# Kernel optimization log

Hardware: AMD Instinct MI355X
Metric: run time of the kernel (lower is better)

The kernel has to match this reference:

```python
import jax, jax.numpy as jnp
import numpy as np

D_MODEL = 1024
NUM_HEADS = 16
D_HEAD = D_MODEL // NUM_HEADS
ROPE_THETA = 10000.0


def _rope(x, pos):
    # x: [..., S, d_head]; rotate consecutive pairs (2i, 2i+1)
    half = x.shape[-1] // 2
    inv_freq = ROPE_THETA ** (-jnp.arange(half, dtype=jnp.float32) * 2.0 / x.shape[-1])
    ang = pos[:, None].astype(jnp.float32) * inv_freq[None, :]  # [S, half]
    cos, sin = jnp.cos(ang), jnp.sin(ang)
    x1, x2 = x[..., 0::2], x[..., 1::2]
    r1 = x1 * cos - x2 * sin
    r2 = x1 * sin + x2 * cos
    return jnp.stack([r1, r2], axis=-1).reshape(x.shape)


def setup_inputs() -> dict:
    key = jax.random.key(0)
    ks = jax.random.split(key, 5)
    s = 1.0 / np.sqrt(D_MODEL)
    return {
        "q_weight": jax.random.normal(ks[0], (D_MODEL, D_MODEL), jnp.float32) * s,
        "k_weight": jax.random.normal(ks[1], (D_MODEL, D_MODEL), jnp.float32) * s,
        "v_weight": jax.random.normal(ks[2], (D_MODEL, D_MODEL), jnp.float32) * s,
        "o_weight": jax.random.normal(ks[3], (D_MODEL, D_MODEL), jnp.float32) * s,
        "in_features": jax.random.normal(ks[4], (2, 2048, D_MODEL), jnp.float32),
    }


def reference(q_weight, k_weight, v_weight, o_weight, in_features):
    S = in_features.shape[-2]
    qw = q_weight.reshape(NUM_HEADS, D_HEAD, D_MODEL)
    kw = k_weight.reshape(NUM_HEADS, D_HEAD, D_MODEL)
    vw = v_weight.reshape(NUM_HEADS, D_HEAD, D_MODEL)
    # [B, H, S, d_head]
    q = jnp.einsum('bsj,nhj->bnsh', in_features, qw)
    k = jnp.einsum('bsj,nhj->bnsh', in_features, kw)
    v = jnp.einsum('bsj,nhj->bnsh', in_features, vw)
    pos = jnp.arange(S)
    q = _rope(q, pos)
    k = _rope(k, pos)
    scale = 1.0 / jnp.sqrt(jnp.asarray(D_HEAD, dtype=q.dtype))
    scores = jnp.einsum('bnqh,bnkh->bnqk', q, k) * scale  # [B,H,S,S]
    causal = jnp.tril(jnp.ones((S, S), dtype=bool))
    scores = jnp.where(causal, scores, jnp.asarray(-jnp.inf, dtype=scores.dtype))
    attn = jax.nn.softmax(scores, axis=-1)
    out = jnp.einsum('bnqk,bnkh->bnqh', attn, v)  # [B,H,S,d_head]
    out = jnp.swapaxes(out, -2, -3).reshape(*out.shape[:-3], S, D_MODEL)
    return jnp.einsum('ji,bki->bkj', o_weight, out)
```

## Files before the change

kernel.cpp:

```cpp
#include <hip/hip_runtime.h>
#include <math.h>

typedef __attribute__((ext_vector_type(8))) short bf16x8;
typedef __attribute__((ext_vector_type(4))) float f32x4;

static constexpr int D_MODEL = 1024;
static constexpr int SEQ = 2048;
static constexpr int BATCH = 2;
static constexpr int M_TOT = BATCH * SEQ;

__device__ __forceinline__ unsigned short f2bf(float f) {
  unsigned int u = __builtin_bit_cast(unsigned int, f);
  u += 0x7fffu + ((u >> 16) & 1u);
  return (unsigned short)(u >> 16);
}

__device__ __forceinline__ void gld16(const unsigned short* g, unsigned short* l) {
  __builtin_amdgcn_global_load_lds(
      (const __attribute__((address_space(1))) unsigned int*)g,
      (__attribute__((address_space(3))) unsigned int*)l, 16, 0, 0);
}

__global__ void cvt_f32_bf16(const float* __restrict__ src,
                             unsigned short* __restrict__ dst, int n4) {
  int i = blockIdx.x * blockDim.x + threadIdx.x;
  if (i >= n4) return;
  const float4 v = reinterpret_cast<const float4*>(src)[i];
  ushort4 o;
  o.x = f2bf(v.x); o.y = f2bf(v.y); o.z = f2bf(v.z); o.w = f2bf(v.w);
  reinterpret_cast<ushort4*>(dst)[i] = o;
}

__global__ void cvt_weights(const float* __restrict__ qw, const float* __restrict__ kw,
                            const float* __restrict__ vw, const float* __restrict__ ow,
                            unsigned short* __restrict__ dst) {
  int i = blockIdx.x * blockDim.x + threadIdx.x;
  const int which = i >> 18;
  const int off = i & 262143;
  const float* src = (which == 0) ? qw : (which == 1) ? kw : (which == 2) ? vw : ow;
  const float4 v = reinterpret_cast<const float4*>(src)[off];
  ushort4 o;
  o.x = f2bf(v.x); o.y = f2bf(v.y); o.z = f2bf(v.z); o.w = f2bf(v.w);
  reinterpret_cast<ushort4*>(dst)[i] = o;
}

__global__ void rope_tables(float2* __restrict__ ct2) {
  int idx = blockIdx.x * blockDim.x + threadIdx.x;
  int s = idx >> 5;
  int p = idx & 31;
  float inv_freq = powf(10000.0f, -(float)p / 32.0f);
  float ang = (float)s * inv_freq;
  int psw = p ^ (((s >> 2) & 1) << 3);
  float2 cs; cs.x = cosf(ang); cs.y = sinf(ang);
  ct2[s * 32 + psw] = cs;
}

template <int BM, int BN, int MODE>
__global__ __launch_bounds__(256, 2)
void gemm2(const unsigned short* __restrict__ A,
           const unsigned short* __restrict__ W,
           unsigned short* __restrict__ Qd,
           unsigned short* __restrict__ Kd,
           unsigned short* __restrict__ Vd,
           float* __restrict__ Fd,
           const float2* __restrict__ ct2) {
  constexpr int MI = BM / 32, NI = BN / 32;
  constexpr int NKT = D_MODEL / 32;
  constexpr int LOADS = BM / 64 + BN / 64;
  __shared__ __align__(16) unsigned short smem[2 * (BM + BN) * 32];
  unsigned short* Asm = smem;
  unsigned short* Bsm = smem + 2 * BM * 32;
  const int tid  = threadIdx.x;
  const int lane = tid & 63;
  const int wave = tid >> 6;
  const int wm = wave >> 1, wn = wave & 1;
  const int m0 = blockIdx.y * BM;
  const int n0 = blockIdx.x * BN;
  const int lr = lane & 15, lg = lane >> 4;

  const int srow = lane >> 2;
  const int scol = ((lane & 3) ^ ((lane >> 3) & 3)) * 8;

  auto stage = [&](int buf, int kt) {
    const int k0 = kt * 32;
#pragma unroll
    for (int rr = 0; rr < BM / 64; ++rr) {
      const int ch = rr * 4 + wave;
      gld16(&A[(size_t)(m0 + ch * 16 + srow) * D_MODEL + k0 + scol], &Asm[buf * BM * 32 + ch * 512]);
    }
#pragma unroll
    for (int rr = 0; rr < BN / 64; ++rr) {
      const int ch = rr * 4 + wave;
      gld16(&W[(size_t)(n0 + ch * 16 + srow) * D_MODEL + k0 + scol], &Bsm[buf * BN * 32 + ch * 512]);
    }
  };

  f32x4 acc[MI][NI] = {};

  stage(0, 0);
  stage(1, 1);
  __builtin_amdgcn_sched_barrier(0);

  const int swz = (lg ^ ((lr >> 1) & 3)) * 8;

  for (int kt = 0; kt < NKT; ++kt) {
    const int cur = kt & 1;
    if (kt + 1 < NKT) {
      if constexpr (LOADS == 4) asm volatile("s_waitcnt vmcnt(4)" ::: "memory");
      else                      asm volatile("s_waitcnt vmcnt(3)" ::: "memory");
    } else {
      asm volatile("s_waitcnt vmcnt(0)" ::: "memory");
    }
    __builtin_amdgcn_s_barrier();
    __builtin_amdgcn_sched_barrier(0);

    bf16x8 af[MI], bfr[NI];
#pragma unroll
    for (int i = 0; i < MI; ++i)
      af[i] = *reinterpret_cast<const bf16x8*>(&Asm[cur * BM * 32 + (wm * (BM / 2) + i * 16 + lr) * 32 + swz]);
#pragma unroll
    for (int j = 0; j < NI; ++j)
      bfr[j] = *reinterpret_cast<const bf16x8*>(&Bsm[cur * BN * 32 + (wn * (BN / 2) + j * 16 + lr) * 32 + swz]);
    asm volatile("s_waitcnt lgkmcnt(0)" ::: "memory");
    __builtin_amdgcn_sched_barrier(0);
    __builtin_amdgcn_s_barrier();
    __builtin_amdgcn_sched_barrier(0);

    if (kt + 2 < NKT) stage(cur, kt + 2);
    __builtin_amdgcn_sched_barrier(0);

#pragma unroll
    for (int i = 0; i < MI; ++i)
#pragma unroll
      for (int j = 0; j < NI; ++j)
        acc[i][j] = __builtin_amdgcn_mfma_f32_16x16x32_bf16(af[i], bfr[j], acc[i][j], 0, 0, 0);
  }

  if constexpr (MODE == 2) {
#pragma unroll
    for (int i = 0; i < MI; ++i)
#pragma unroll
      for (int j = 0; j < NI; ++j)
#pragma unroll
        for (int r = 0; r < 4; ++r) {
          const int gm = m0 + wm * (BM / 2) + i * 16 + lg * 4 + r;
          const int gc = n0 + wn * (BN / 2) + j * 16 + lr;
          Fd[(size_t)gm * D_MODEL + gc] = acc[i][j][r];
        }
  } else {
    const int t = n0 >> 10;
    const int b = m0 >> 11;
    const int s_base = m0 & 2047;
    if (t < 2) {
      unsigned short* dstQ = (t == 0) ? Qd : Kd;
      const unsigned short* gsrc = (const unsigned short*)(ct2 + (size_t)s_base * 32);
#pragma unroll
      for (int it = 0; it < 8; ++it) {
        const int ch = wave * 8 + it;
        gld16(&gsrc[ch * 512 + lane * 8], &smem[ch * 512]);
      }
      asm volatile("s_waitcnt vmcnt(0)" ::: "memory");
      __builtin_amdgcn_sched_barrier(0);
      __builtin_amdgcn_s_barrier();
      const float2* tbl = (const float2*)smem;
      const int nbase = (n0 & 1023) >> 6;
#pragma unroll
      for (int i = 0; i < MI; ++i) {
#pragma unroll
        for (int j = 0; j < NI; ++j) {
#pragma unroll
          for (int r = 0; r < 4; ++r) {
            const int sl = wm * (BM / 2) + i * 16 + lg * 4 + r;
            const int h  = j * 16 + lr;
            const int psw = (h >> 1) ^ (((sl >> 2) & 1) << 3);
            const float2 cs = tbl[sl * 32 + psw];
            float x = acc[i][j][r];
            const float part = __shfl_xor(x, 1, 64);
            x = (h & 1) ? (part * cs.y + x * cs.x) : (x * cs.x - part * cs.y);
            const int n = nbase + wn;
            dstQ[(size_t)((b * 16 + n) * SEQ + s_base + sl) * 64 + h] = f2bf(x);
          }
        }
      }
    } else {
      unsigned short* tile = smem;
      const int row = tid >> 2;
      const int ck  = tid & 3;
      for (int pass = 0; pass < 2; ++pass) {
        __builtin_amdgcn_s_barrier();
        if (wn == pass) {
#pragma unroll
          for (int i = 0; i < MI; ++i)
#pragma unroll
            for (int j = 0; j < NI; ++j)
#pragma unroll
              for (int r = 0; r < 4; ++r)
                tile[(j * 16 + lr) * 136 + wm * 64 + i * 16 + lg * 4 + r] = f2bf(acc[i][j][r]);
        }
        asm volatile("s_waitcnt lgkmcnt(0)" ::: "memory");
        __builtin_amdgcn_sched_barrier(0);
        __builtin_amdgcn_s_barrier();
        const int c = (n0 & 1023) + pass * 64 + row;
        const int n = c >> 6, h = c & 63;
        unsigned short* vrow = &Vd[(size_t)((b * 16 + n) * 64 + h) * SEQ + s_base + ck * 32];
        const unsigned short* lrow = &tile[row * 136 + ck * 32];
#pragma unroll
        for (int k = 0; k < 4; ++k)
          *reinterpret_cast<bf16x8*>(&vrow[k * 8]) = *reinterpret_cast<const bf16x8*>(&lrow[k * 8]);
      }
    }
  }
}

__global__ __launch_bounds__(256, 2)
void attn_kernel(const unsigned short* __restrict__ Q,
                 const unsigned short* __restrict__ K,
                 const unsigned short* __restrict__ Vt,
                 unsigned short* __restrict__ AO) {
  __shared__ __align__(16) unsigned short Ksh[2][4096];
  __shared__ __align__(16) unsigned short Vsh[2][4096];
  __shared__ unsigned short Pl[4][32 * 72];
  const int bn   = blockIdx.x;
  const int j    = (gridDim.y - 1) - blockIdx.y;
  const int wave = threadIdx.x >> 6;
  const int lane = threadIdx.x & 63;
  const int lr = lane & 15, lg = lane >> 4;
  const int q0 = j * 128 + wave * 32;
  const unsigned short* Qh = Q  + (size_t)bn * SEQ * 64;
  const unsigned short* Kh = K  + (size_t)bn * SEQ * 64;
  const unsigned short* Vh = Vt + (size_t)bn * 64 * SEQ;
  unsigned short* Pw = &Pl[wave][0];
  const int b = bn >> 4, n = bn & 15;

  const int srow8 = lane >> 3;
  const int scolb = ((lane & 7) ^ srow8) * 8;

  auto stage = [&](int buf, int k0) {
#pragma unroll
    for (int c = 0; c < 2; ++c) {
      const int ch = wave * 2 + c;
      const int row = ch * 8 + srow8;
      gld16(&Kh[(size_t)(k0 + row) * 64 + scolb], &Ksh[buf][ch * 512]);
      gld16(&Vh[(size_t)row * SEQ + k0 + scolb], &Vsh[buf][ch * 512]);
    }
  };

  constexpr float KL2E = 0.125f * 1.44269504088896f;
  const int nt = 2 * j + 2;

  bf16x8 qf[2][2];
#pragma unroll
  for (int mi = 0; mi < 2; ++mi)
#pragma unroll
    for (int ks = 0; ks < 2; ++ks)
      qf[mi][ks] = *reinterpret_cast<const bf16x8*>(
          &Qh[(size_t)(q0 + mi * 16 + lr) * 64 + ks * 32 + lg * 8]);
  asm volatile("s_waitcnt vmcnt(0)" ::: "memory");
  __builtin_amdgcn_sched_barrier(0);

  f32x4 o[2][4] = {};
  float lsum[2][4] = {};

  stage(0, 0);
  stage(1, 64);
  __builtin_amdgcn_sched_barrier(0);

  for (int t = 0; t < nt; ++t) {
    const int cur = t & 1;
    const int k0 = t * 64;
    if (t + 1 < nt) { asm volatile("s_waitcnt vmcnt(4)" ::: "memory"); }
    else            { asm volatile("s_waitcnt vmcnt(0)" ::: "memory"); }
    __builtin_amdgcn_s_barrier();
    __builtin_amdgcn_sched_barrier(0);

    const unsigned short* Kc = &Ksh[cur][0];
    const unsigned short* Vc = &Vsh[cur][0];

    bf16x8 kf[4][2];
#pragma unroll
    for (int nj = 0; nj < 4; ++nj)
#pragma unroll
      for (int ks = 0; ks < 2; ++ks) {
        const int R = nj * 16 + lr;
        const int p = (ks * 4 + lg) ^ (R & 7);
        kf[nj][ks] = *reinterpret_cast<const bf16x8*>(&Kc[R * 64 + p * 8]);
      }
    f32x4 sf[2][4] = {};
    __builtin_amdgcn_s_setprio(1);
#pragma unroll
    for (int nj = 0; nj < 4; ++nj)
#pragma unroll
      for (int ks = 0; ks < 2; ++ks)
#pragma unroll
        for (int mi = 0; mi < 2; ++mi)
          sf[mi][nj] = __builtin_amdgcn_mfma_f32_16x16x32_bf16(qf[mi][ks], kf[nj][ks], sf[mi][nj], 0, 0, 0);
    __builtin_amdgcn_s_setprio(0);

    if (k0 + 63 <= q0) {
#pragma unroll
      for (int mi = 0; mi < 2; ++mi)
#pragma unroll
        for (int nj = 0; nj < 4; ++nj)
#pragma unroll
          for (int r = 0; r < 4; ++r) {
            const float p = __builtin_amdgcn_exp2f(sf[mi][nj][r] * KL2E);
            lsum[mi][r] += p;
            Pw[(mi * 16 + lg * 4 + r) * 72 + nj * 16 + lr] = f2bf(p);
          }
    } else {
#pragma unroll
      for (int mi = 0; mi < 2; ++mi)
#pragma unroll
        for (int nj = 0; nj < 4; ++nj)
#pragma unroll
          for (int r = 0; r < 4; ++r) {
            const int qrow = q0 + mi * 16 + lg * 4 + r;
            const int kcol = k0 + nj * 16 + lr;
            const float p = (kcol <= qrow) ? __builtin_amdgcn_exp2f(sf[mi][nj][r] * KL2E) : 0.0f;
            lsum[mi][r] += p;
            Pw[(mi * 16 + lg * 4 + r) * 72 + nj * 16 + lr] = f2bf(p);
          }
    }

    bf16x8 vf[2][4];
#pragma unroll
    for (int ks2 = 0; ks2 < 2; ++ks2)
#pragma unroll
      for (int hf = 0; hf < 4; ++hf) {
        const int R = hf * 16 + lr;
        const int p = (ks2 * 4 + lg) ^ (R & 7);
        vf[ks2][hf] = *reinterpret_cast<const bf16x8*>(&Vc[R * 64 + p * 8]);
      }
    asm volatile("s_waitcnt lgkmcnt(0)" ::: "memory");
    __builtin_amdgcn_sched_barrier(0);
    __builtin_amdgcn_s_barrier();
    __builtin_amdgcn_sched_barrier(0);

    if (t + 2 < nt) stage(cur, (t + 2) * 64);
    __builtin_amdgcn_sched_barrier(0);

    bf16x8 pf[2][2];
#pragma unroll
    for (int mi = 0; mi < 2; ++mi)
#pragma unroll
      for (int ks2 = 0; ks2 < 2; ++ks2)
        pf[mi][ks2] = *reinterpret_cast<const bf16x8*>(&Pw[(mi * 16 + lr) * 72 + ks2 * 32 + lg * 8]);
    __builtin_amdgcn_s_setprio(1);
#pragma unroll
    for (int ks2 = 0; ks2 < 2; ++ks2)
#pragma unroll
      for (int hf = 0; hf < 4; ++hf)
#pragma unroll
        for (int mi = 0; mi < 2; ++mi)
          o[mi][hf] = __builtin_amdgcn_mfma_f32_16x16x32_bf16(pf[mi][ks2], vf[ks2][hf], o[mi][hf], 0, 0, 0);
    __builtin_amdgcn_s_setprio(0);
  }

#pragma unroll
  for (int mi = 0; mi < 2; ++mi)
#pragma unroll
    for (int r = 0; r < 4; ++r) {
      float s = lsum[mi][r];
#pragma unroll
      for (int d = 1; d < 16; d <<= 1) s += __shfl_xor(s, d, 64);
      const float inv = 1.0f / s;
      const int srow = q0 + mi * 16 + lg * 4 + r;
#pragma unroll
      for (int hf = 0; hf < 4; ++hf) {
        const int h = hf * 16 + lr;
        AO[(size_t)(b * SEQ + srow) * D_MODEL + n * 64 + h] = f2bf(o[mi][hf][r] * inv);
      }
    }
}

extern "C" void kernel_launch(void* const* d_in, const int* in_sizes, int n_in,
                              void* d_out, int out_size, void* d_ws, size_t ws_size,
                              hipStream_t stream) {
  const float* qw = (const float*)d_in[0];
  const float* kw = (const float*)d_in[1];
  const float* vw = (const float*)d_in[2];
  const float* ow = (const float*)d_in[3];
  const float* x  = (const float*)d_in[4];

  char* ws = (char*)d_ws;
  const size_t XB = (size_t)M_TOT * D_MODEL * 2;
  const size_t WB = (size_t)D_MODEL * D_MODEL * 2;
  unsigned short* Xb  = (unsigned short*)ws;  ws += XB;
  unsigned short* Wqb = (unsigned short*)ws;  ws += WB;
  unsigned short* Wkb = (unsigned short*)ws;  ws += WB;
  unsigned short* Wvb = (unsigned short*)ws;  ws += WB;
  unsigned short* Wob = (unsigned short*)ws;  ws += WB;
  unsigned short* Qr  = (unsigned short*)ws;  ws += XB;
  unsigned short* Kr  = (unsigned short*)ws;  ws += XB;
  unsigned short* Vt  = (unsigned short*)ws;  ws += XB;
  unsigned short* AO  = (unsigned short*)ws;  ws += XB;
  float2* ct2 = (float2*)ws;  ws += (size_t)SEQ * 32 * 8;
  (void)Wkb; (void)Wvb;

  cvt_f32_bf16<<<(M_TOT * D_MODEL / 4) / 256, 256, 0, stream>>>(x, Xb, M_TOT * D_MODEL / 4);
  cvt_weights<<<(4 * D_MODEL * D_MODEL / 4) / 256, 256, 0, stream>>>(qw, kw, vw, ow, Wqb);
  rope_tables<<<(SEQ * 32) / 256, 256, 0, stream>>>(ct2);

  gemm2<128, 128, 0><<<dim3(3072 / 128, M_TOT / 128), 256, 0, stream>>>(
      Xb, Wqb, Qr, Kr, Vt, nullptr, ct2);

  attn_kernel<<<dim3(BATCH * 16, 16), 256, 0, stream>>>(Qr, Kr, Vt, AO);

  gemm2<128, 64, 2><<<dim3(D_MODEL / 64, M_TOT / 128), 256, 0, stream>>>(
      AO, Wob, nullptr, nullptr, nullptr, (float*)d_out, nullptr);
}
```

Before: 115.5 us.

## Transpose QK^T MFMA operands to pack P writes with bf16 pair converts

Swaps the MFMA operand order for the score computation so each lane holds four consecutive key columns of one query row. P is then converted with packed v_cvt_pk_bf16_f32 and written to LDS as 8-byte stores, and the row sums shrink to one accumulator per row group, reduced with cross-lane shuffles at the end. The softmax/P-store block also moves after the V fragment loads so the LDS reads can overlap the exp work. This cuts scalar bf16 rounding, LDS store count and register pressure, at the cost of inline asm that blocks compiler scheduling.

```diff
diff --git a/kernel.cpp b/kernel.cpp
--- a/kernel.cpp
+++ b/kernel.cpp
@@ -3,6 +3,7 @@
 
 typedef __attribute__((ext_vector_type(8))) short bf16x8;
 typedef __attribute__((ext_vector_type(4))) float f32x4;
+typedef __attribute__((ext_vector_type(2))) unsigned int u32x2;
 
 static constexpr int D_MODEL = 1024;
 static constexpr int SEQ = 2048;
@@ -13,6 +14,12 @@
   unsigned int u = __builtin_bit_cast(unsigned int, f);
   u += 0x7fffu + ((u >> 16) & 1u);
   return (unsigned short)(u >> 16);
+}
+
+__device__ __forceinline__ unsigned int cvtpk(float lo, float hi) {
+  unsigned int r;
+  asm volatile("v_cvt_pk_bf16_f32 %0, %1, %2" : "=v"(r) : "v"(lo), "v"(hi));
+  return r;
 }
 
 __device__ __forceinline__ void gld16(const unsigned short* g, unsigned short* l) {
@@ -219,7 +226,7 @@
                  unsigned short* __restrict__ AO) {
   __shared__ __align__(16) unsigned short Ksh[2][4096];
   __shared__ __align__(16) unsigned short Vsh[2][4096];
-  __shared__ unsigned short Pl[4][32 * 72];
+  __shared__ __align__(16) unsigned short Pl[4][32 * 72];
   const int bn   = blockIdx.x;
   const int j    = (gridDim.y - 1) - blockIdx.y;
   const int wave = threadIdx.x >> 6;
@@ -259,7 +266,7 @@
   __builtin_amdgcn_sched_barrier(0);
 
   f32x4 o[2][4] = {};
-  float lsum[2][4] = {};
+  float ls[2] = {0.f, 0.f};
 
   stage(0, 0);
   stage(1, 64);
@@ -293,34 +300,8 @@
       for (int ks = 0; ks < 2; ++ks)
 #pragma unroll
         for (int mi = 0; mi < 2; ++mi)
-          sf[mi][nj] = __builtin_amdgcn_mfma_f32_16x16x32_bf16(qf[mi][ks], kf[nj][ks], sf[mi][nj], 0, 0, 0);
+          sf[mi][nj] = __builtin_amdgcn_mfma_f32_16x16x32_bf16(kf[nj][ks], qf[mi][ks], sf[mi][nj], 0, 0, 0);
     __builtin_amdgcn_s_setprio(0);
-
-    if (k0 + 63 <= q0) {
-#pragma unroll
-      for (int mi = 0; mi < 2; ++mi)
-#pragma unroll
-        for (int nj = 0; nj < 4; ++nj)
-#pragma unroll
-          for (int r = 0; r < 4; ++r) {
-            const float p = __builtin_amdgcn_exp2f(sf[mi][nj][r] * KL2E);
-            lsum[mi][r] += p;
-            Pw[(mi * 16 + lg * 4 + r) * 72 + nj * 16 + lr] = f2bf(p);
-          }
-    } else {
-#pragma unroll
-      for (int mi = 0; mi < 2; ++mi)
-#pragma unroll
-        for (int nj = 0; nj < 4; ++nj)
-#pragma unroll
-          for (int r = 0; r < 4; ++r) {
-            const int qrow = q0 + mi * 16 + lg * 4 + r;
-            const int kcol = k0 + nj * 16 + lr;
-            const float p = (kcol <= qrow) ? __builtin_amdgcn_exp2f(sf[mi][nj][r] * KL2E) : 0.0f;
-            lsum[mi][r] += p;
-            Pw[(mi * 16 + lg * 4 + r) * 72 + nj * 16 + lr] = f2bf(p);
-          }
-    }
 
     bf16x8 vf[2][4];
 #pragma unroll
@@ -331,6 +312,38 @@
         const int p = (ks2 * 4 + lg) ^ (R & 7);
         vf[ks2][hf] = *reinterpret_cast<const bf16x8*>(&Vc[R * 64 + p * 8]);
       }
+
+    if (k0 + 63 <= q0) {
+#pragma unroll
+      for (int mi = 0; mi < 2; ++mi)
+#pragma unroll
+        for (int nj = 0; nj < 4; ++nj) {
+          const float p0 = __builtin_amdgcn_exp2f(sf[mi][nj][0] * KL2E);
+          const float p1 = __builtin_amdgcn_exp2f(sf[mi][nj][1] * KL2E);
+          const float p2 = __builtin_amdgcn_exp2f(sf[mi][nj][2] * KL2E);
+          const float p3 = __builtin_amdgcn_exp2f(sf[mi][nj][3] * KL2E);
+          ls[mi] += (p0 + p1) + (p2 + p3);
+          u32x2 w; w[0] = cvtpk(p0, p1); w[1] = cvtpk(p2, p3);
+          *reinterpret_cast<u32x2*>(&Pw[(mi * 16 + lr) * 72 + nj * 16 + lg * 4]) = w;
+        }
+    } else {
+#pragma unroll
+      for (int mi = 0; mi < 2; ++mi) {
+        const int qrow = q0 + mi * 16 + lr;
+#pragma unroll
+        for (int nj = 0; nj < 4; ++nj) {
+          const int kb = k0 + nj * 16 + lg * 4;
+          float p[4];
+#pragma unroll
+          for (int r = 0; r < 4; ++r)
+            p[r] = (kb + r <= qrow) ? __builtin_amdgcn_exp2f(sf[mi][nj][r] * KL2E) : 0.0f;
+          ls[mi] += (p[0] + p[1]) + (p[2] + p[3]);
+          u32x2 w; w[0] = cvtpk(p[0], p[1]); w[1] = cvtpk(p[2], p[3]);
+          *reinterpret_cast<u32x2*>(&Pw[(mi * 16 + lr) * 72 + nj * 16 + lg * 4]) = w;
+        }
+      }
+    }
+
     asm volatile("s_waitcnt lgkmcnt(0)" ::: "memory");
     __builtin_amdgcn_sched_barrier(0);
     __builtin_amdgcn_s_barrier();
@@ -357,13 +370,18 @@
   }
 
 #pragma unroll
+  for (int mi = 0; mi < 2; ++mi) {
+    float s = ls[mi];
+    s += __shfl_xor(s, 16, 64);
+    s += __shfl_xor(s, 32, 64);
+    ls[mi] = s;
+  }
+#pragma unroll
   for (int mi = 0; mi < 2; ++mi)
 #pragma unroll
     for (int r = 0; r < 4; ++r) {
-      float s = lsum[mi][r];
-#pragma unroll
-      for (int d = 1; d < 16; d <<= 1) s += __shfl_xor(s, d, 64);
-      const float inv = 1.0f / s;
+      const float sv = __shfl(ls[mi], lg * 4 + r, 64);
+      const float inv = 1.0f / sv;
       const int srow = q0 + mi * 16 + lg * 4 + r;
 #pragma unroll
       for (int hf = 0; hf < 4; ++hf) {
```

After: 105.6 us. -8.5%, faster.
